# Performance work log

Hardware: AMD Instinct MI355X
Metric: run time of the kernel (lower is better)

## Reference

```python
import jax, jax.numpy as jnp
import numpy as np
import math

EMBED_DIM = 768
NUM_HEADS = 12


def setup_inputs() -> dict:
    key = jax.random.key(0)
    ks = jax.random.split(key, 5)
    R, C, B, E = 128, 256, 1, EMBED_DIM
    s = 1.0 / math.sqrt(E)
    x = jax.random.normal(ks[0], (R, C, B, E), dtype=jnp.float32)
    wq = jax.random.normal(ks[1], (E, E), dtype=jnp.float32) * s
    wk = jax.random.normal(ks[2], (E, E), dtype=jnp.float32) * s
    wv = jax.random.normal(ks[3], (E, E), dtype=jnp.float32) * s
    wo = jax.random.normal(ks[4], (E, E), dtype=jnp.float32) * s
    z = jnp.zeros((E,), dtype=jnp.float32)
    return {"x": x, "wq": wq, "bq": z, "wk": wk, "bk": z,
            "wv": wv, "bv": z, "wo": wo, "bo": z}


def reference(x, wq, bq, wk, bk, wv, bv, wo, bo):
    R, C, B, E = x.shape
    H = NUM_HEADS
    D = E // H
    shape = (R, C, B, H, D)
    # tied row attention scaling: 1/sqrt(head_dim) * 1/sqrt(num_rows)
    scaling = (D ** -0.5) / math.sqrt(R)
    q = jnp.reshape(x @ wq + bq, shape) * scaling
    k = jnp.reshape(x @ wk + bk, shape)
    v = jnp.reshape(x @ wv + bv, shape)
    # logits summed (tied) over the row axis r: [H, B, C, C]
    attn_weights = jnp.einsum('rinhd,rjnhd->hnij', q, k)
    attn_probs = jax.nn.softmax(attn_weights, axis=-1)
    # broadcast probs back to every row
    context = jnp.einsum('hnij,rjnhd->rinhd', attn_probs, v)
    context = jnp.reshape(context, (R, C, B, E))
    return context @ wo + bo
```

## Files before the change

kernel.cpp:

```cpp
#include <hip/hip_runtime.h>
#include <hip/hip_bf16.h>
#include <math.h>

typedef __bf16 bf16_t;
typedef __bf16 vbf4 __attribute__((ext_vector_type(4)));
typedef __bf16 vbf8 __attribute__((ext_vector_type(8)));
typedef float  vf4  __attribute__((ext_vector_type(4)));

#define OFF_XB   0ull
#define OFF_Q    50331648ull
#define OFF_K    100663296ull
#define OFF_VT   150994944ull
#define OFF_P    201326592ull
#define OFF_WQ   202899456ull
#define OFF_WK   204079104ull
#define OFF_WV   205258752ull
#define OFF_WO   206438400ull

__device__ __forceinline__ int xcd_swizzle(int bid, int per_xcd) {
  return (bid & 7) * per_xcd + (bid >> 3);
}

template <int ROWS>
__device__ __forceinline__ void stage_tile(const bf16_t* __restrict__ g,
                                           int ld, int row0, int k0,
                                           bf16_t* lds, int tid) {
  const int wave = tid >> 6;
  const int lane = tid & 63;
  const int js = (lane & 7) ^ (lane >> 3);
#pragma unroll
  for (int cc = 0; cc < ROWS / 32; ++cc) {
    const int chunk = cc * 4 + wave;
    const int row = chunk * 8 + (lane >> 3);
    const bf16_t* gp = g + (size_t)(row0 + row) * ld + k0 + js * 8;
    bf16_t* lp = lds + chunk * 512 + lane * 8;
    __builtin_amdgcn_global_load_lds(
        (const __attribute__((address_space(1))) void*)gp,
        (__attribute__((address_space(3))) void*)lp, 16, 0, 0);
  }
}

__device__ __forceinline__ vbf8 lds_frag(const bf16_t* s, int rr, int ko) {
  const int c = (ko >> 3) ^ (rr & 7);
  return *(const vbf8*)&s[rr * 64 + (c << 3)];
}

__device__ __forceinline__ void gemm_mainloop128(const bf16_t* __restrict__ A, int lda, int m0,
                                                 const bf16_t* __restrict__ Bt, int ldb, int n0,
                                                 int kbeg, int kend,
                                                 bf16_t* As, bf16_t* Bs,
                                                 vf4 (&acc)[4][4]) {
  const int tid = threadIdx.x;
  const int lane = tid & 63;
  const int wave = tid >> 6;
  const int wm0 = (wave >> 1) * 64;
  const int wn0 = (wave & 1) * 64;
  const int fm = lane & 15;
  const int fk = (lane >> 4) * 8;
  for (int k0 = kbeg; k0 < kend; k0 += 64) {
    stage_tile<128>(A, lda, m0, k0, As, tid);
    stage_tile<128>(Bt, ldb, n0, k0, Bs, tid);
    __syncthreads();
#pragma unroll
    for (int kk = 0; kk < 64; kk += 32) {
      vbf8 af[4], bfv[4];
#pragma unroll
      for (int mt = 0; mt < 4; ++mt) af[mt] = lds_frag(As, wm0 + mt * 16 + fm, kk + fk);
#pragma unroll
      for (int nt = 0; nt < 4; ++nt) bfv[nt] = lds_frag(Bs, wn0 + nt * 16 + fm, kk + fk);
#pragma unroll
      for (int mt = 0; mt < 4; ++mt)
#pragma unroll
        for (int nt = 0; nt < 4; ++nt)
          acc[mt][nt] = __builtin_amdgcn_mfma_f32_16x16x32_bf16(af[mt], bfv[nt],
                                                                acc[mt][nt], 0, 0, 0);
    }
    __syncthreads();
  }
}

__device__ __forceinline__ void zero_acc4(vf4 (&acc)[4][4]) {
  const vf4 z = {0.f, 0.f, 0.f, 0.f};
#pragma unroll
  for (int mt = 0; mt < 4; ++mt)
#pragma unroll
    for (int nt = 0; nt < 4; ++nt) acc[mt][nt] = z;
}

__global__ __launch_bounds__(256) void pack_x(const float* __restrict__ x,
                                              bf16_t* __restrict__ Xb) {
  const size_t idx = (size_t)blockIdx.x * 256 + threadIdx.x;
  const float4 v = ((const float4*)x)[idx];
  vbf4 o;
  o[0] = (bf16_t)v.x; o[1] = (bf16_t)v.y; o[2] = (bf16_t)v.z; o[3] = (bf16_t)v.w;
  ((vbf4*)Xb)[idx] = o;
}

__global__ __launch_bounds__(256) void pack_w(const float* __restrict__ wq,
                                              const float* __restrict__ wk,
                                              const float* __restrict__ wv,
                                              const float* __restrict__ wo,
                                              bf16_t* __restrict__ Wq, bf16_t* __restrict__ Wk,
                                              bf16_t* __restrict__ Wv, bf16_t* __restrict__ Wo,
                                              float scaling) {
  __shared__ float t[64][65];
  const int wid = blockIdx.y;
  const float* src = (wid == 0) ? wq : (wid == 1) ? wk : (wid == 2) ? wv : wo;
  bf16_t* dst = (wid == 0) ? Wq : (wid == 1) ? Wk : (wid == 2) ? Wv : Wo;
  const float sc = (wid == 0) ? scaling : 1.0f;
  const int kt = (blockIdx.x / 12) * 64;
  const int nt = (blockIdx.x % 12) * 64;
  const int tx = threadIdx.x & 63;
  const int ty = threadIdx.x >> 6;
#pragma unroll
  for (int p = 0; p < 16; ++p) {
    const int k = ty + p * 4;
    t[tx][k] = src[(size_t)(kt + k) * 768 + nt + tx] * sc;
  }
  __syncthreads();
#pragma unroll
  for (int p = 0; p < 16; ++p) {
    const int n = ty + p * 4;
    dst[(size_t)(nt + n) * 768 + kt + tx] = (bf16_t)t[n][tx];
  }
}

__global__ __launch_bounds__(256, 3) void qkv_gemm(const bf16_t* __restrict__ Xb,
                                                   const bf16_t* __restrict__ Wq,
                                                   const bf16_t* __restrict__ Wk,
                                                   const bf16_t* __restrict__ Wv,
                                                   const float* __restrict__ bq,
                                                   const float* __restrict__ bk,
                                                   const float* __restrict__ bv,
                                                   bf16_t* __restrict__ Qh,
                                                   bf16_t* __restrict__ Kh,
                                                   bf16_t* __restrict__ Vt,
                                                   float scaling) {
  __shared__ __align__(16) bf16_t As[128 * 64];
  __shared__ __align__(16) bf16_t Bs[128 * 64];
  const int bx = xcd_swizzle(blockIdx.x, 576);
  const int m_idx = bx / 18;
  const int rem = bx - m_idx * 18;
  const int n_idx = rem / 3;
  const int z = rem - n_idx * 3;
  const int m0 = m_idx * 128;
  const int n0 = n_idx * 128;
  const bf16_t* W = (z == 0) ? Wq : (z == 1) ? Wk : Wv;
  vf4 acc[4][4];
  zero_acc4(acc);
  gemm_mainloop128(Xb, 768, m0, W, 768, n0, 0, 768, As, Bs, acc);

  const int lane = threadIdx.x & 63;
  const int wave = threadIdx.x >> 6;
  const int wm0 = (wave >> 1) * 64;
  const int wn0 = (wave & 1) * 64;
  const int col = lane & 15;
  const int rq = (lane >> 4) * 4;
  const float* bias = (z == 0) ? bq : (z == 1) ? bk : bv;
  const float bsc = (z == 0) ? scaling : 1.0f;

  if (z < 2) {
    bf16_t* O = (z == 0) ? Qh : Kh;
#pragma unroll
    for (int mt = 0; mt < 4; ++mt) {
#pragma unroll
      for (int nt = 0; nt < 4; ++nt) {
        const int n = n0 + wn0 + nt * 16 + col;
        const int h = n >> 6, d = n & 63;
        const float bb = bias[n] * bsc;
#pragma unroll
        for (int i = 0; i < 4; ++i) {
          const int m = m0 + wm0 + mt * 16 + rq + i;
          const int r = m >> 8, c = m & 255;
          O[(size_t)(h * 256 + c) * 8192 + (r << 6) + d] = (bf16_t)(acc[mt][nt][i] + bb);
        }
      }
    }
  } else {
#pragma unroll
    for (int mt = 0; mt < 4; ++mt) {
      const int mb = m0 + wm0 + mt * 16 + rq;
      const int r = mb >> 8, c = mb & 255;
#pragma unroll
      for (int nt = 0; nt < 4; ++nt) {
        const int n = n0 + wn0 + nt * 16 + col;
        const int h = n >> 6, d = n & 63;
        const float bb = bias[n];
        vbf4 pk;
#pragma unroll
        for (int i = 0; i < 4; ++i) pk[i] = (bf16_t)(acc[mt][nt][i] + bb);
        *(vbf4*)&Vt[(size_t)h * 2097152 + ((size_t)((r << 6) + d)) * 256 + c] = pk;
      }
    }
  }
}

__global__ __launch_bounds__(256, 3) void logits_gemm(const bf16_t* __restrict__ Qh,
                                                      const bf16_t* __restrict__ Kh,
                                                      float* __restrict__ Lp) {
  __shared__ __align__(16) bf16_t As[128 * 64];
  __shared__ __align__(16) bf16_t Bs[128 * 64];
  const int bx = xcd_swizzle(blockIdx.x, 96);
  const int z = bx >> 2;
  const int h = z >> 4;
  const int kseg = z & 15;
  const int m0 = ((bx >> 1) & 1) * 128;
  const int n0 = (bx & 1) * 128;
  const bf16_t* A = Qh + (size_t)h * (256 * 8192);
  const bf16_t* B = Kh + (size_t)h * (256 * 8192);
  vf4 acc[4][4];
  zero_acc4(acc);
  gemm_mainloop128(A, 8192, m0, B, 8192, n0, kseg * 512, kseg * 512 + 512, As, Bs, acc);

  const int lane = threadIdx.x & 63;
  const int wave = threadIdx.x >> 6;
  const int wm0 = (wave >> 1) * 64;
  const int wn0 = (wave & 1) * 64;
  const int col = lane & 15;
  const int rq = (lane >> 4) * 4;
  float* Lph = Lp + ((size_t)(kseg * 12 + h)) * 65536;
#pragma unroll
  for (int mt = 0; mt < 4; ++mt)
#pragma unroll
    for (int nt = 0; nt < 4; ++nt) {
      const int n = n0 + wn0 + nt * 16 + col;
#pragma unroll
      for (int i = 0; i < 4; ++i) {
        const int m = m0 + wm0 + mt * 16 + rq + i;
        Lph[(size_t)m * 256 + n] = acc[mt][nt][i];
      }
    }
}

__global__ __launch_bounds__(256) void softmax_k(const float* __restrict__ Lp,
                                                 bf16_t* __restrict__ P) {
  const int row = blockIdx.x * 4 + (threadIdx.x >> 6);
  const int lane = threadIdx.x & 63;
  float a = 0.f, b = 0.f, c = 0.f, d = 0.f;
#pragma unroll
  for (int ks = 0; ks < 16; ++ks) {
    const float4 v4 = ((const float4*)(Lp + (size_t)ks * 786432 + (size_t)row * 256))[lane];
    a += v4.x; b += v4.y; c += v4.z; d += v4.w;
  }
  float mx = fmaxf(fmaxf(a, b), fmaxf(c, d));
#pragma unroll
  for (int off = 32; off; off >>= 1) mx = fmaxf(mx, __shfl_xor(mx, off));
  a = expf(a - mx); b = expf(b - mx); c = expf(c - mx); d = expf(d - mx);
  float s = a + b + c + d;
#pragma unroll
  for (int off = 32; off; off >>= 1) s += __shfl_xor(s, off);
  const float inv = 1.0f / s;
  vbf4 o;
  o[0] = (bf16_t)(a * inv); o[1] = (bf16_t)(b * inv);
  o[2] = (bf16_t)(c * inv); o[3] = (bf16_t)(d * inv);
  ((vbf4*)(P + (size_t)row * 256))[lane] = o;
}

__global__ __launch_bounds__(256, 3) void ctx_gemm(const bf16_t* __restrict__ P,
                                                   const bf16_t* __restrict__ Vt,
                                                   bf16_t* __restrict__ CtxTok) {
  __shared__ __align__(16) bf16_t As[128 * 64];
  __shared__ __align__(16) bf16_t Bs[128 * 64];
  const int bx = xcd_swizzle(blockIdx.x, 192);
  const int h = bx >> 7;
  const int rem = bx & 127;
  const int n0 = (rem >> 1) * 128;
  const int m0 = (rem & 1) * 128;
  const bf16_t* A = P + (size_t)h * 65536;
  const bf16_t* B = Vt + (size_t)h * 2097152;
  vf4 acc[4][4];
  zero_acc4(acc);
  gemm_mainloop128(A, 256, m0, B, 256, n0, 0, 256, As, Bs, acc);

  const int lane = threadIdx.x & 63;
  const int wave = threadIdx.x >> 6;
  const int wm0 = (wave >> 1) * 64;
  const int wn0 = (wave & 1) * 64;
  const int col = lane & 15;
  const int rq = (lane >> 4) * 4;
#pragma unroll
  for (int mt = 0; mt < 4; ++mt)
#pragma unroll
    for (int nt = 0; nt < 4; ++nt) {
      const int n = n0 + wn0 + nt * 16 + col;
      const int r = n >> 6, d = n & 63;
#pragma unroll
      for (int i = 0; i < 4; ++i) {
        const int m = m0 + wm0 + mt * 16 + rq + i;
        CtxTok[(size_t)((r << 8) + m) * 768 + (h << 6) + d] = (bf16_t)acc[mt][nt][i];
      }
    }
}

__global__ __launch_bounds__(256, 3) void out_gemm(const bf16_t* __restrict__ Ctx,
                                                   const bf16_t* __restrict__ Wo,
                                                   const float* __restrict__ bo,
                                                   float* __restrict__ Out) {
  __shared__ __align__(16) bf16_t As[128 * 64];
  __shared__ __align__(16) bf16_t Bs[128 * 64];
  const int bx = xcd_swizzle(blockIdx.x, 192);
  const int m_idx = bx / 6;
  const int n_idx = bx - m_idx * 6;
  const int m0 = m_idx * 128;
  const int n0 = n_idx * 128;
  vf4 acc[4][4];
  zero_acc4(acc);
  gemm_mainloop128(Ctx, 768, m0, Wo, 768, n0, 0, 768, As, Bs, acc);

  const int lane = threadIdx.x & 63;
  const int wave = threadIdx.x >> 6;
  const int wm0 = (wave >> 1) * 64;
  const int wn0 = (wave & 1) * 64;
  const int col = lane & 15;
  const int rq = (lane >> 4) * 4;
#pragma unroll
  for (int mt = 0; mt < 4; ++mt)
#pragma unroll
    for (int nt = 0; nt < 4; ++nt) {
      const int n = n0 + wn0 + nt * 16 + col;
      const float bb = bo[n];
#pragma unroll
      for (int i = 0; i < 4; ++i) {
        const int m = m0 + wm0 + mt * 16 + rq + i;
        Out[(size_t)m * 768 + n] = acc[mt][nt][i] + bb;
      }
    }
}

extern "C" void kernel_launch(void* const* d_in, const int* in_sizes, int n_in,
                              void* d_out, int out_size, void* d_ws, size_t ws_size,
                              hipStream_t stream) {
  const float* x  = (const float*)d_in[0];
  const float* wq = (const float*)d_in[1];
  const float* bq = (const float*)d_in[2];
  const float* wk = (const float*)d_in[3];
  const float* bk = (const float*)d_in[4];
  const float* wv = (const float*)d_in[5];
  const float* bv = (const float*)d_in[6];
  const float* wo = (const float*)d_in[7];
  const float* bo = (const float*)d_in[8];
  float* out = (float*)d_out;

  char* ws = (char*)d_ws;
  bf16_t* Xb  = (bf16_t*)(ws + OFF_XB);
  float*  Lp  = (float*)(ws + OFF_XB);
  bf16_t* Ctx = (bf16_t*)(ws + OFF_XB);
  bf16_t* Qh  = (bf16_t*)(ws + OFF_Q);
  bf16_t* Kh  = (bf16_t*)(ws + OFF_K);
  bf16_t* Vt  = (bf16_t*)(ws + OFF_VT);
  bf16_t* P   = (bf16_t*)(ws + OFF_P);
  bf16_t* Wq  = (bf16_t*)(ws + OFF_WQ);
  bf16_t* Wk  = (bf16_t*)(ws + OFF_WK);
  bf16_t* Wv  = (bf16_t*)(ws + OFF_WV);
  bf16_t* Wo  = (bf16_t*)(ws + OFF_WO);

  const float scaling = 0.125f / sqrtf(128.0f);

  pack_x<<<24576, 256, 0, stream>>>(x, Xb);
  pack_w<<<dim3(144, 4), 256, 0, stream>>>(wq, wk, wv, wo, Wq, Wk, Wv, Wo, scaling);
  qkv_gemm<<<4608, 256, 0, stream>>>(Xb, Wq, Wk, Wv, bq, bk, bv, Qh, Kh, Vt, scaling);
  logits_gemm<<<768, 256, 0, stream>>>(Qh, Kh, Lp);
  softmax_k<<<768, 256, 0, stream>>>(Lp, P);
  ctx_gemm<<<1536, 256, 0, stream>>>(P, Vt, Ctx);
  out_gemm<<<1536, 256, 0, stream>>>(Ctx, Wo, bo, out);

  (void)in_sizes; (void)n_in; (void)out_size; (void)ws_size;
}
```

Before: 415.2 us.

## Fuse pack kernels, enlarge logits tile to 256x256, store partials in bf16

Merges the x and weight packing kernels into one launch. Rewrites the logits GEMM to use 512-thread blocks that each compute a full 256x256 head tile per K segment, so Q and K tiles are loaded once instead of twice. The split-K partial logits are now written and read as bf16 instead of fp32, halving that traffic, at the cost of precision in the partial sums before softmax. The grid shrinks to 192 blocks, which may underfill the GPU.

```diff
diff --git a/kernel.cpp b/kernel.cpp
--- a/kernel.cpp
+++ b/kernel.cpp
@@ -33,6 +33,24 @@
     const int chunk = cc * 4 + wave;
     const int row = chunk * 8 + (lane >> 3);
     const bf16_t* gp = g + (size_t)(row0 + row) * ld + k0 + js * 8;
+    bf16_t* lp = lds + chunk * 512 + lane * 8;
+    __builtin_amdgcn_global_load_lds(
+        (const __attribute__((address_space(1))) void*)gp,
+        (__attribute__((address_space(3))) void*)lp, 16, 0, 0);
+  }
+}
+
+__device__ __forceinline__ void stage_tile512_256(const bf16_t* __restrict__ g,
+                                                  int ld, int k0,
+                                                  bf16_t* lds, int tid) {
+  const int wave = tid >> 6;
+  const int lane = tid & 63;
+  const int js = (lane & 7) ^ (lane >> 3);
+#pragma unroll
+  for (int cc = 0; cc < 4; ++cc) {
+    const int chunk = cc * 8 + wave;
+    const int row = chunk * 8 + (lane >> 3);
+    const bf16_t* gp = g + (size_t)row * ld + k0 + js * 8;
     bf16_t* lp = lds + chunk * 512 + lane * 8;
     __builtin_amdgcn_global_load_lds(
         (const __attribute__((address_space(1))) void*)gp,
@@ -87,29 +105,33 @@
     for (int nt = 0; nt < 4; ++nt) acc[mt][nt] = z;
 }
 
-__global__ __launch_bounds__(256) void pack_x(const float* __restrict__ x,
-                                              bf16_t* __restrict__ Xb) {
-  const size_t idx = (size_t)blockIdx.x * 256 + threadIdx.x;
-  const float4 v = ((const float4*)x)[idx];
-  vbf4 o;
-  o[0] = (bf16_t)v.x; o[1] = (bf16_t)v.y; o[2] = (bf16_t)v.z; o[3] = (bf16_t)v.w;
-  ((vbf4*)Xb)[idx] = o;
-}
-
-__global__ __launch_bounds__(256) void pack_w(const float* __restrict__ wq,
-                                              const float* __restrict__ wk,
-                                              const float* __restrict__ wv,
-                                              const float* __restrict__ wo,
-                                              bf16_t* __restrict__ Wq, bf16_t* __restrict__ Wk,
-                                              bf16_t* __restrict__ Wv, bf16_t* __restrict__ Wo,
-                                              float scaling) {
+__global__ __launch_bounds__(256) void pack_all(const float* __restrict__ x,
+                                                const float* __restrict__ wq,
+                                                const float* __restrict__ wk,
+                                                const float* __restrict__ wv,
+                                                const float* __restrict__ wo,
+                                                bf16_t* __restrict__ Xb,
+                                                bf16_t* __restrict__ Wq, bf16_t* __restrict__ Wk,
+                                                bf16_t* __restrict__ Wv, bf16_t* __restrict__ Wo,
+                                                float scaling) {
   __shared__ float t[64][65];
-  const int wid = blockIdx.y;
+  const int bid = blockIdx.x;
+  if (bid < 24576) {
+    const size_t idx = (size_t)bid * 256 + threadIdx.x;
+    const float4 v = ((const float4*)x)[idx];
+    vbf4 o;
+    o[0] = (bf16_t)v.x; o[1] = (bf16_t)v.y; o[2] = (bf16_t)v.z; o[3] = (bf16_t)v.w;
+    ((vbf4*)Xb)[idx] = o;
+    return;
+  }
+  const int wb = bid - 24576;
+  const int wid = wb / 144;
+  const int tile = wb - wid * 144;
   const float* src = (wid == 0) ? wq : (wid == 1) ? wk : (wid == 2) ? wv : wo;
   bf16_t* dst = (wid == 0) ? Wq : (wid == 1) ? Wk : (wid == 2) ? Wv : Wo;
   const float sc = (wid == 0) ? scaling : 1.0f;
-  const int kt = (blockIdx.x / 12) * 64;
-  const int nt = (blockIdx.x % 12) * 64;
+  const int kt = (tile / 12) * 64;
+  const int nt = (tile % 12) * 64;
   const int tx = threadIdx.x & 63;
   const int ty = threadIdx.x >> 6;
 #pragma unroll
@@ -195,52 +217,79 @@
   }
 }
 
-__global__ __launch_bounds__(256, 3) void logits_gemm(const bf16_t* __restrict__ Qh,
+__global__ __launch_bounds__(512, 2) void logits_gemm(const bf16_t* __restrict__ Qh,
                                                       const bf16_t* __restrict__ Kh,
-                                                      float* __restrict__ Lp) {
-  __shared__ __align__(16) bf16_t As[128 * 64];
-  __shared__ __align__(16) bf16_t Bs[128 * 64];
-  const int bx = xcd_swizzle(blockIdx.x, 96);
-  const int z = bx >> 2;
-  const int h = z >> 4;
-  const int kseg = z & 15;
-  const int m0 = ((bx >> 1) & 1) * 128;
-  const int n0 = (bx & 1) * 128;
+                                                      bf16_t* __restrict__ Lp) {
+  __shared__ __align__(16) bf16_t As[256 * 64];
+  __shared__ __align__(16) bf16_t Bs[256 * 64];
+  const int bx = xcd_swizzle(blockIdx.x, 24);
+  const int h = bx >> 4;
+  const int kseg = bx & 15;
   const bf16_t* A = Qh + (size_t)h * (256 * 8192);
   const bf16_t* B = Kh + (size_t)h * (256 * 8192);
-  vf4 acc[4][4];
-  zero_acc4(acc);
-  gemm_mainloop128(A, 8192, m0, B, 8192, n0, kseg * 512, kseg * 512 + 512, As, Bs, acc);
-
-  const int lane = threadIdx.x & 63;
-  const int wave = threadIdx.x >> 6;
-  const int wm0 = (wave >> 1) * 64;
-  const int wn0 = (wave & 1) * 64;
+
+  const int tid = threadIdx.x;
+  const int lane = tid & 63;
+  const int wave = tid >> 6;
+  const int aRow0 = (wave >> 2) * 128;
+  const int bRow0 = (wave & 3) * 64;
+  const int fm = lane & 15;
+  const int fk = (lane >> 4) * 8;
+
+  vf4 acc[8][4];
+  const vf4 z4 = {0.f, 0.f, 0.f, 0.f};
+#pragma unroll
+  for (int mt = 0; mt < 8; ++mt)
+#pragma unroll
+    for (int nt = 0; nt < 4; ++nt) acc[mt][nt] = z4;
+
+  const int kbeg = kseg * 512;
+  for (int k0 = kbeg; k0 < kbeg + 512; k0 += 64) {
+    stage_tile512_256(A, 8192, k0, As, tid);
+    stage_tile512_256(B, 8192, k0, Bs, tid);
+    __syncthreads();
+#pragma unroll
+    for (int kk = 0; kk < 64; kk += 32) {
+      vbf8 af[8], bfv[4];
+#pragma unroll
+      for (int mt = 0; mt < 8; ++mt) af[mt] = lds_frag(As, aRow0 + mt * 16 + fm, kk + fk);
+#pragma unroll
+      for (int nt = 0; nt < 4; ++nt) bfv[nt] = lds_frag(Bs, bRow0 + nt * 16 + fm, kk + fk);
+#pragma unroll
+      for (int mt = 0; mt < 8; ++mt)
+#pragma unroll
+        for (int nt = 0; nt < 4; ++nt)
+          acc[mt][nt] = __builtin_amdgcn_mfma_f32_16x16x32_bf16(af[mt], bfv[nt],
+                                                                acc[mt][nt], 0, 0, 0);
+    }
+    __syncthreads();
+  }
+
   const int col = lane & 15;
   const int rq = (lane >> 4) * 4;
-  float* Lph = Lp + ((size_t)(kseg * 12 + h)) * 65536;
-#pragma unroll
-  for (int mt = 0; mt < 4; ++mt)
+  bf16_t* Lph = Lp + ((size_t)(kseg * 12 + h)) * 65536;
+#pragma unroll
+  for (int mt = 0; mt < 8; ++mt)
 #pragma unroll
     for (int nt = 0; nt < 4; ++nt) {
-      const int n = n0 + wn0 + nt * 16 + col;
+      const int n = bRow0 + nt * 16 + col;
 #pragma unroll
       for (int i = 0; i < 4; ++i) {
-        const int m = m0 + wm0 + mt * 16 + rq + i;
-        Lph[(size_t)m * 256 + n] = acc[mt][nt][i];
+        const int m = aRow0 + mt * 16 + rq + i;
+        Lph[(size_t)m * 256 + n] = (bf16_t)acc[mt][nt][i];
       }
     }
 }
 
-__global__ __launch_bounds__(256) void softmax_k(const float* __restrict__ Lp,
+__global__ __launch_bounds__(256) void softmax_k(const bf16_t* __restrict__ Lp,
                                                  bf16_t* __restrict__ P) {
   const int row = blockIdx.x * 4 + (threadIdx.x >> 6);
   const int lane = threadIdx.x & 63;
   float a = 0.f, b = 0.f, c = 0.f, d = 0.f;
 #pragma unroll
   for (int ks = 0; ks < 16; ++ks) {
-    const float4 v4 = ((const float4*)(Lp + (size_t)ks * 786432 + (size_t)row * 256))[lane];
-    a += v4.x; b += v4.y; c += v4.z; d += v4.w;
+    const vbf4 v4 = ((const vbf4*)(Lp + (size_t)ks * 786432 + (size_t)row * 256))[lane];
+    a += (float)v4[0]; b += (float)v4[1]; c += (float)v4[2]; d += (float)v4[3];
   }
   float mx = fmaxf(fmaxf(a, b), fmaxf(c, d));
 #pragma unroll
@@ -343,7 +392,7 @@
 
   char* ws = (char*)d_ws;
   bf16_t* Xb  = (bf16_t*)(ws + OFF_XB);
-  float*  Lp  = (float*)(ws + OFF_XB);
+  bf16_t* Lp  = (bf16_t*)(ws + OFF_XB);
   bf16_t* Ctx = (bf16_t*)(ws + OFF_XB);
   bf16_t* Qh  = (bf16_t*)(ws + OFF_Q);
   bf16_t* Kh  = (bf16_t*)(ws + OFF_K);
@@ -356,10 +405,9 @@
 
   const float scaling = 0.125f / sqrtf(128.0f);
 
-  pack_x<<<24576, 256, 0, stream>>>(x, Xb);
-  pack_w<<<dim3(144, 4), 256, 0, stream>>>(wq, wk, wv, wo, Wq, Wk, Wv, Wo, scaling);
+  pack_all<<<25152, 256, 0, stream>>>(x, wq, wk, wv, wo, Xb, Wq, Wk, Wv, Wo, scaling);
   qkv_gemm<<<4608, 256, 0, stream>>>(Xb, Wq, Wk, Wv, bq, bk, bv, Qh, Kh, Vt, scaling);
-  logits_gemm<<<768, 256, 0, stream>>>(Qh, Kh, Lp);
+  logits_gemm<<<192, 512, 0, stream>>>(Qh, Kh, Lp);
   softmax_k<<<768, 256, 0, stream>>>(Lp, P);
   ctx_gemm<<<1536, 256, 0, stream>>>(P, Vt, Ctx);
   out_gemm<<<1536, 256, 0, stream>>>(Ctx, Wo, bo, out);
```

Result: slower. 431.0 us (+3.8%).
